# Optimization experiments

Measured on AMD Instinct MI355X. Metric: run time of the kernel, lower is better.

The kernel has to match this reference:

```python
import jax, jax.numpy as jnp
import numpy as np

B, S, D, O, E = 8, 4096, 1024, 1024, 64

def setup_inputs() -> dict:
    key = jax.random.key(0)
    kx, kgw, kgb, kew, keb = jax.random.split(key, 5)
    x = jax.random.normal(kx, (B, S, D), dtype=jnp.float32)
    gate_w = jax.random.normal(kgw, (E, D), dtype=jnp.float32) * 0.02
    gate_b = jnp.zeros((E,), dtype=jnp.float32)
    expert_w = jax.random.normal(kew, (E, D, O), dtype=jnp.float32) * 0.02
    expert_b = jnp.zeros((E, O), dtype=jnp.float32)
    return {"x": x, "gate_w": gate_w, "gate_b": gate_b,
            "expert_w": expert_w, "expert_b": expert_b}

def reference(x, gate_w, gate_b, expert_w, expert_b):
    # x: [B,S,D] -> flatten tokens. With world_size=1 the all-reduce and
    # all-to-alls in the torch module are identities, and per-chunk processing
    # is token-independent, so one global pass is mathematically identical.
    b, s, d = x.shape
    xt = x.reshape(-1, d)                                   # [N, D]
    logits = xt @ gate_w.T + gate_b                         # [N, E]
    gates = jax.nn.softmax(logits, axis=-1)
    sel = jnp.argmax(gates, axis=-1)                        # [N] top-1 expert
    order = jnp.argsort(sel)                                # stable sort by expert
    xs = xt[order]                                          # tokens grouped by expert
    counts = jnp.bincount(sel, length=E).astype(jnp.int32)  # tokens per expert
    # Grouped expert GEMM: row block e of xs multiplies expert_w[e].
    ys = jax.lax.ragged_dot(xs, expert_w, counts)           # [N, O]
    ys = ys + expert_b[sel[order]]
    # Combine: scatter sorted outputs back to original token positions.
    # (Note: torch output is NOT scaled by gate probability.)
    out = jnp.zeros((xt.shape[0], expert_w.shape[-1]), dtype=ys.dtype)
    out = out.at[order].set(ys)
    return out.reshape(b, s, -1)
```

## Files before the change

### kernel.cpp

```cpp
#include <hip/hip_runtime.h>
#include <hip/hip_bf16.h>

#define N_TOK 32768
#define DIM 1024
#define OUTD 1024
#define NEXP 64

typedef __attribute__((ext_vector_type(4))) float f32x4;
typedef __attribute__((ext_vector_type(8))) short bf16x8;

__device__ __forceinline__ unsigned short f2bf(float f) {
    unsigned int u = __builtin_bit_cast(unsigned int, f);
    u += 0x7FFFu + ((u >> 16) & 1u);
    return (unsigned short)(u >> 16);
}

__device__ __forceinline__ uint4 pack8(float4 a, float4 b) {
    uint4 p;
    p.x = (unsigned int)f2bf(a.x) | ((unsigned int)f2bf(a.y) << 16);
    p.y = (unsigned int)f2bf(a.z) | ((unsigned int)f2bf(a.w) << 16);
    p.z = (unsigned int)f2bf(b.x) | ((unsigned int)f2bf(b.y) << 16);
    p.w = (unsigned int)f2bf(b.z) | ((unsigned int)f2bf(b.w) << 16);
    return p;
}

__device__ __forceinline__ float4 ntload4(const float* p) {
    f32x4 v = __builtin_nontemporal_load(reinterpret_cast<const f32x4*>(p));
    float4 r; r.x = v[0]; r.y = v[1]; r.z = v[2]; r.w = v[3];
    return r;
}

#define GLOAD16(gp, lp) \
    __builtin_amdgcn_global_load_lds((const __attribute__((address_space(1))) void*)(gp), \
                                     (__attribute__((address_space(3))) void*)(lp), 16, 0, 0)

__global__ __launch_bounds__(256) void prep_kernel(const float* __restrict__ x,
        const float* __restrict__ gw, const float* __restrict__ gb,
        const float* __restrict__ ew,
        int* __restrict__ sel, int* __restrict__ nflag, int* __restrict__ flags,
        int* __restrict__ counts,
        unsigned short* __restrict__ xb, unsigned short* __restrict__ wt)
{
    __shared__ __align__(16) char smem[18688];
    int tid = threadIdx.x;

    if (blockIdx.x < 512) {
        unsigned short* Ag = (unsigned short*)smem;
        unsigned short* Bg = (unsigned short*)(smem + 8192);
        int* h = (int*)(smem + 16384);
        if (tid < NEXP) h[tid] = 0;

        int t0 = blockIdx.x * 64;
        int lane = tid & 63;
        int w = tid >> 6;
        int lr = lane & 15, lg = lane >> 4;

        int rowS = tid >> 2;
        int koffS = (((tid & 3) ^ ((tid >> 3) & 3)) * 8);
        const float* xsrc = x + (size_t)(t0 + rowS) * DIM + koffS;
        const float* wsrc = gw + (size_t)rowS * DIM + koffS;
        unsigned short* xdst = xb ? xb + (size_t)(t0 + rowS) * DIM + koffS : nullptr;

        f32x4 acc[4];
#pragma unroll
        for (int n = 0; n < 4; n++)
#pragma unroll
            for (int c = 0; c < 4; c++) acc[n][c] = 0.f;

        float4 v0 = *reinterpret_cast<const float4*>(xsrc);
        float4 v1 = *reinterpret_cast<const float4*>(xsrc + 4);
        float4 v2 = *reinterpret_cast<const float4*>(wsrc);
        float4 v3 = *reinterpret_cast<const float4*>(wsrc + 4);
        {
            uint4 pa = pack8(v0, v1), pb = pack8(v2, v3);
            *reinterpret_cast<uint4*>(&Ag[tid * 8]) = pa;
            *reinterpret_cast<uint4*>(&Bg[tid * 8]) = pb;
            if (xdst) *reinterpret_cast<uint4*>(xdst) = pa;
        }
        __syncthreads();

        const char* Agc = (const char*)Ag;
        const char* Bgc = (const char*)Bg;
        int fko = (lg ^ ((lr >> 1) & 3)) * 16;

#pragma unroll 1
        for (int t = 0; t < 32; ++t) {
            if (t < 31) {
                int k0 = (t + 1) * 32;
                v0 = *reinterpret_cast<const float4*>(xsrc + k0);
                v1 = *reinterpret_cast<const float4*>(xsrc + k0 + 4);
                v2 = *reinterpret_cast<const float4*>(wsrc + k0);
                v3 = *reinterpret_cast<const float4*>(wsrc + k0 + 4);
            }
            int boff = (t & 1) * 4096;
            bf16x8 afr = *reinterpret_cast<const bf16x8*>(Agc + boff + ((w * 16 + lr) << 6) + fko);
#pragma unroll
            for (int n = 0; n < 4; n++) {
                bf16x8 bfr = *reinterpret_cast<const bf16x8*>(Bgc + boff + ((n * 16 + lr) << 6) + fko);
                acc[n] = __builtin_amdgcn_mfma_f32_16x16x32_bf16(afr, bfr, acc[n], 0, 0, 0);
            }
            if (t < 31) {
                uint4 pa = pack8(v0, v1), pb = pack8(v2, v3);
                int soff = ((t + 1) & 1) * 2048;
                *reinterpret_cast<uint4*>(&Ag[soff + tid * 8]) = pa;
                *reinterpret_cast<uint4*>(&Bg[soff + tid * 8]) = pb;
                if (xdst) *reinterpret_cast<uint4*>(xdst + (t + 1) * 32) = pa;
            }
            __syncthreads();
        }

        float gbv[4];
#pragma unroll
        for (int n = 0; n < 4; n++) gbv[n] = gb[n * 16 + lr];
#pragma unroll
        for (int i = 0; i < 4; i++) {
            float m1 = -1e30f, m2 = -1e30f; int e1 = 0;
#pragma unroll
            for (int n = 0; n < 4; n++) {
                float v = acc[n][i] + gbv[n];
                if (v > m1) { m2 = m1; m1 = v; e1 = n * 16 + lr; }
                else if (v > m2) m2 = v;
            }
#pragma unroll
            for (int d = 1; d < 16; d <<= 1) {
                float om1 = __shfl_xor(m1, d, 16);
                float om2 = __shfl_xor(m2, d, 16);
                int   oe1 = __shfl_xor(e1, d, 16);
                if (om1 > m1 || (om1 == m1 && oe1 < e1)) {
                    m2 = fmaxf(om2, m1); m1 = om1; e1 = oe1;
                } else {
                    m2 = fmaxf(m2, om1);
                }
            }
            if (lr == 0) {
                int t = t0 + w * 16 + lg * 4 + i;
                sel[t] = e1;
                atomicAdd(&h[e1], 1);
                if (m1 - m2 < 0.01f) {
                    int idx = atomicAdd(nflag, 1);
                    if (idx < 16384) flags[idx] = t;
                }
            }
        }
        __syncthreads();
        if (tid < NEXP && h[tid]) atomicAdd(&counts[tid], h[tid]);
    } else {
        if (!wt) return;
        unsigned short* ts0 = (unsigned short*)smem;
        unsigned short* ts1 = (unsigned short*)(smem + 9216);
        int lin = blockIdx.x - 512;
        int e = lin >> 5;
        int d0 = ((lin >> 4) & 1) * 512;
        int o0 = (lin & 15) * 64;
        const float* src = ew + (size_t)e * (DIM * OUTD);
        unsigned short* dst = wt + (size_t)e * (DIM * OUTD);
        int og = tid & 7;
        int dl = tid >> 3;
        int dc = tid & 7;
        int ol = tid >> 3;

        float4 c0, c1, c2, c3;
        {
            const float* sr0 = &src[(size_t)(d0 + dl) * OUTD + o0 + og * 8];
            const float* sr1 = &src[(size_t)(d0 + dl + 32) * OUTD + o0 + og * 8];
            c0 = ntload4(sr0);
            c1 = ntload4(sr0 + 4);
            c2 = ntload4(sr1);
            c3 = ntload4(sr1 + 4);
        }
#pragma unroll
        for (int s = 0; s < 8; ++s) {
            float4 n0 = c0, n1 = c1, n2 = c2, n3 = c3;
            if (s < 7) {
                int dsn = d0 + (s + 1) * 64;
                const float* sr0 = &src[(size_t)(dsn + dl) * OUTD + o0 + og * 8];
                const float* sr1 = &src[(size_t)(dsn + dl + 32) * OUTD + o0 + og * 8];
                n0 = ntload4(sr0);
                n1 = ntload4(sr0 + 4);
                n2 = ntload4(sr1);
                n3 = ntload4(sr1 + 4);
            }
            unsigned short* tsb = (s & 1) ? ts1 : ts0;
#pragma unroll
            for (int half = 0; half < 2; ++half) {
                int dLoc = dl + 32 * half;
                float4 va = half ? c2 : c0;
                float4 vb = half ? c3 : c1;
                unsigned short b[8] = { f2bf(va.x), f2bf(va.y), f2bf(va.z), f2bf(va.w),
                                        f2bf(vb.x), f2bf(vb.y), f2bf(vb.z), f2bf(vb.w) };
                int dg = dLoc >> 3, dr = dLoc & 7;
#pragma unroll
                for (int k = 0; k < 8; k++) {
                    int o = og * 8 + k;
                    int key = (o & 7) ^ ((o >> 3) & 7);
                    tsb[o * 72 + ((dg ^ key) << 3) + dr] = b[k];
                }
            }
            __syncthreads();
            int ds0 = d0 + s * 64;
#pragma unroll
            for (int i = 0; i < 2; i++) {
                int o = ol + 32 * i;
                int key = (o & 7) ^ ((o >> 3) & 7);
                uint4 v = *reinterpret_cast<const uint4*>(&tsb[o * 72 + ((dc ^ key) << 3)]);
                *reinterpret_cast<uint4*>(&dst[(size_t)(o0 + o) * DIM + ds0 + dc * 8]) = v;
            }
            c0 = n0; c1 = n1; c2 = n2; c3 = n3;
        }
    }
}

__global__ __launch_bounds__(256) void gate_fix_kernel(const float* __restrict__ x,
        const float* __restrict__ gw, const float* __restrict__ gb,
        int* __restrict__ sel, const int* __restrict__ nflag, const int* __restrict__ flags,
        int* __restrict__ counts)
{
    __shared__ __align__(16) float xrow[4][DIM];
    int n = *nflag; if (n > 16384) n = 16384;
    int wv = threadIdx.x >> 6, lane = threadIdx.x & 63;
    int fi = blockIdx.x * 4 + wv;
    if (fi >= n) return;
    int t = flags[fi];

    const float4* xs4 = reinterpret_cast<const float4*>(x + (size_t)t * DIM);
    float4* xl4 = reinterpret_cast<float4*>(xrow[wv]);
#pragma unroll
    for (int i = 0; i < 4; i++)
        xl4[lane + i * 64] = xs4[lane + i * 64];

    const float4* wr4 = reinterpret_cast<const float4*>(gw + (size_t)lane * DIM);
    double a0 = 0, a1 = 0, a2 = 0, a3 = 0;
#pragma unroll 4
    for (int k = 0; k < DIM / 4; ++k) {
        float4 wv4 = wr4[k];
        float4 xv4 = xl4[k];
        a0 += (double)xv4.x * (double)wv4.x;
        a1 += (double)xv4.y * (double)wv4.y;
        a2 += (double)xv4.z * (double)wv4.z;
        a3 += (double)xv4.w * (double)wv4.w;
    }
    double m1 = ((a0 + a1) + (a2 + a3)) + (double)gb[lane];
    int e1 = lane;
#pragma unroll
    for (int d = 1; d < 64; d <<= 1) {
        double om1 = __shfl_xor(m1, d, 64);
        int   oe1  = __shfl_xor(e1, d, 64);
        if (om1 > m1 || (om1 == m1 && oe1 < e1)) { m1 = om1; e1 = oe1; }
    }
    if (lane == 0) {
        int eOld = sel[t];
        if (eOld != e1) {
            sel[t] = e1;
            atomicSub(&counts[eOld], 1);
            atomicAdd(&counts[e1], 1);
        }
    }
}

__global__ void sched_kernel(const int* __restrict__ counts, int* __restrict__ offsets,
                             int* __restrict__ schedE, int* __restrict__ schedR,
                             int* __restrict__ totalRB, int rowsShift)
{
    int e = threadIdx.x;
    int c = counts[e];
    int v = c;
#pragma unroll
    for (int d = 1; d < 64; d <<= 1) { int y = __shfl_up(v, d, 64); if (e >= d) v += y; }
    offsets[e] = v - c;
    if (e == 63) offsets[NEXP] = v;
    int rows = 1 << rowsShift;
    int nb = (c + rows - 1) >> rowsShift;
    int rbv = nb;
#pragma unroll
    for (int d = 1; d < 64; d <<= 1) { int y = __shfl_up(rbv, d, 64); if (e >= d) rbv += y; }
    int rbBase = rbv - nb;
    for (int i = 0; i < nb; i++) { schedE[rbBase + i] = e; schedR[rbBase + i] = i << rowsShift; }
    if (e == 63) *totalRB = rbv;
}

__global__ __launch_bounds__(256) void scatter_kernel(const int* __restrict__ sel,
        const int* __restrict__ offsets, int* __restrict__ cursor, int* __restrict__ perm)
{
    int t = blockIdx.x * 256 + threadIdx.x;
    int e = sel[t];
    int pos = offsets[e] + atomicAdd(&cursor[e], 1);
    perm[pos] = t;
}

__global__ __launch_bounds__(512, 4) void moe_gemm7(
        const unsigned short* __restrict__ xb, const unsigned short* __restrict__ wt,
        const float* __restrict__ eb,
        const int* __restrict__ perm, const int* __restrict__ offsets,
        const int* __restrict__ counts, const int* __restrict__ schedE,
        const int* __restrict__ schedR, const int* __restrict__ totalRB,
        float* __restrict__ out)
{
    int idx = blockIdx.x;
    int xcd = idx & 7;
    int s = idx >> 3;
    int cb = s & 7;
    int rb = (s >> 3) * 8 + xcd;
    if (rb >= *totalRB) return;
    int e = schedE[rb], r0 = schedR[rb];
    int cnt = counts[e], base = offsets[e];

    __shared__ __align__(16) unsigned short As[24576];
    __shared__ __align__(16) unsigned short Bs[12288];

    int tid = threadIdx.x;
    int lane = tid & 63;
    int wv = tid >> 6;
    int wr = wv >> 1, wc = wv & 1;
    int lr = lane & 15, lg = lane >> 4;

    int rowS = tid >> 2;
    int koff = ((tid & 3) ^ ((tid >> 3) & 3)) * 8;
    int rA1 = r0 + rowS, rA2 = r0 + 128 + rowS;
    int tokA1 = (rA1 < cnt) ? perm[base + rA1] : 0;
    int tokA2 = (rA2 < cnt) ? perm[base + rA2] : 0;

    const unsigned short* wte = wt + ((size_t)e << 20);
    const unsigned short* aSrc1 = xb + (size_t)tokA1 * DIM + koff;
    const unsigned short* aSrc2 = xb + (size_t)tokA2 * DIM + koff;
    const unsigned short* bSrc1 = wte + (size_t)(cb * 128 + rowS) * DIM + koff;

    unsigned short* AsQ0 = As + wv * 512;
    unsigned short* AsQ1 = As + 4096 + wv * 512;
    unsigned short* BsQ0 = Bs + wv * 512;

    f32x4 acc[4][4];
#pragma unroll
    for (int m = 0; m < 4; m++)
#pragma unroll
        for (int n = 0; n < 4; n++)
#pragma unroll
            for (int c = 0; c < 4; c++) acc[m][n][c] = 0.f;

    const char* Asc = (const char*)As;
    const char* Bsc = (const char*)Bs;
    int fko = (lg ^ ((lr >> 1) & 3)) * 16;

    auto stage = [&](int buf, int k0) {
        GLOAD16(aSrc1 + k0, AsQ0 + buf * 8192);
        GLOAD16(aSrc2 + k0, AsQ1 + buf * 8192);
        GLOAD16(bSrc1 + k0, BsQ0 + buf * 4096);
    };
    auto compute = [&](int buf) {
        int aoff = buf * 16384;
        int boff = buf * 8192;
        bf16x8 bfr[4];
#pragma unroll
        for (int n = 0; n < 4; n++) {
            int row = wc * 64 + n * 16 + lr;
            bfr[n] = *reinterpret_cast<const bf16x8*>(Bsc + boff + (row << 6) + fko);
        }
        __builtin_amdgcn_s_setprio(1);
#pragma unroll
        for (int m = 0; m < 4; m++) {
            int row = wr * 64 + m * 16 + lr;
            bf16x8 afr = *reinterpret_cast<const bf16x8*>(Asc + aoff + (row << 6) + fko);
#pragma unroll
            for (int n = 0; n < 4; n++)
                acc[m][n] = __builtin_amdgcn_mfma_f32_16x16x32_bf16(afr, bfr[n], acc[m][n], 0, 0, 0);
        }
        __builtin_amdgcn_s_setprio(0);
    };

    stage(0, 0);
    stage(1, 32);

    int cbuf = 0, sbuf = 2;
#pragma unroll 1
    for (int t = 0; t < 30; ++t) {
        asm volatile("s_waitcnt vmcnt(3)" ::: "memory");
        __builtin_amdgcn_s_barrier();
        stage(sbuf, (t + 2) * 32);
        compute(cbuf);
        cbuf = (cbuf == 2) ? 0 : cbuf + 1;
        sbuf = (sbuf == 2) ? 0 : sbuf + 1;
    }
    asm volatile("s_waitcnt vmcnt(3)" ::: "memory");
    __builtin_amdgcn_s_barrier();
    compute(cbuf);
    cbuf = (cbuf == 2) ? 0 : cbuf + 1;
    asm volatile("s_waitcnt vmcnt(0)" ::: "memory");
    __builtin_amdgcn_s_barrier();
    compute(cbuf);

    float bias[4];
#pragma unroll
    for (int n = 0; n < 4; n++)
        bias[n] = eb[e * OUTD + cb * 128 + wc * 64 + n * 16 + lr];
#pragma unroll
    for (int m = 0; m < 4; m++) {
        int rowLoc = wr * 64 + m * 16 + lg * 4;
#pragma unroll
        for (int i2 = 0; i2 < 4; i2++) {
            int r = r0 + rowLoc + i2;
            if (r < cnt) {
                int tk = perm[base + r];
                float* op = out + (size_t)tk * OUTD + cb * 128 + wc * 64 + lr;
#pragma unroll
                for (int n = 0; n < 4; n++)
                    __builtin_nontemporal_store(acc[m][n][i2] + bias[n], op + n * 16);
            }
        }
    }
}

extern "C" void kernel_launch(void* const* d_in, const int* in_sizes, int n_in,
                              void* d_out, int out_size, void* d_ws, size_t ws_size,
                              hipStream_t stream)
{
    const float* x  = (const float*)d_in[0];
    const float* gw = (const float*)d_in[1];
    const float* gb = (const float*)d_in[2];
    const float* ew = (const float*)d_in[3];
    const float* eb = (const float*)d_in[4];
    float* out = (float*)d_out;

    char* ws = (char*)d_ws;
    int* counts  = (int*)(ws + 0);
    int* cursor  = (int*)(ws + 256);
    int* offsets = (int*)(ws + 512);
    int* totalRB = (int*)(ws + 1024);
    int* nflag   = (int*)(ws + 1028);
    int* schedE  = (int*)(ws + 2048);
    int* schedR  = (int*)(ws + 4096);
    int* flags   = (int*)(ws + 8192);
    int* sel     = (int*)(ws + 131072);
    int* perm    = (int*)(ws + 262144);

    const size_t WT_OFF   = (size_t)1 << 20;
    const size_t WT_BYTES = (size_t)NEXP * DIM * OUTD * 2;
    const size_t XB_OFF   = WT_OFF + WT_BYTES;
    const size_t XB_BYTES = (size_t)N_TOK * DIM * 2;
    int mode = (ws_size >= XB_OFF + XB_BYTES) ? 2 : 0;
    unsigned short* wt = (mode == 2) ? (unsigned short*)(ws + WT_OFF) : nullptr;
    unsigned short* xb = (mode == 2) ? (unsigned short*)(ws + XB_OFF) : nullptr;

    hipMemsetAsync(ws, 0, 2048, stream);

    prep_kernel<<<dim3(512 + ((mode == 2) ? 2048 : 0)), 256, 0, stream>>>(
        x, gw, gb, ew, sel, nflag, flags, counts, xb, wt);
    gate_fix_kernel<<<dim3(4096), 256, 0, stream>>>(x, gw, gb, sel, nflag, flags, counts);
    sched_kernel<<<dim3(1), 64, 0, stream>>>(counts, offsets, schedE, schedR, totalRB, 8);
    scatter_kernel<<<dim3(N_TOK / 256), 256, 0, stream>>>(sel, offsets, cursor, perm);

    moe_gemm7<<<dim3(1536), 512, 0, stream>>>(xb, wt, eb, perm, offsets, counts,
                                              schedE, schedR, totalRB, out);
}
```

Before: 367.2 us.

## Enlarge GEMM block tile to 256x256 with 1024 threads and 4-stage pipeline

Doubles the output column tile per block to 256, using 16 waves in a 4x4 layout, so each A tile is reused across more columns and the grid shrinks. The LDS ring grows from three to four stages, with one A and one B load per thread per stage and adjusted wait counts. The larger LDS footprint limits each CU to one block, which reduces latency hiding across blocks and leaves fewer blocks to balance uneven expert sizes.

```diff
diff --git a/kernel.cpp b/kernel.cpp
--- a/kernel.cpp
+++ b/kernel.cpp
@@ -287,7 +287,7 @@
     perm[pos] = t;
 }
 
-__global__ __launch_bounds__(512, 4) void moe_gemm7(
+__global__ __launch_bounds__(1024, 4) void moe_gemm10(
         const unsigned short* __restrict__ xb, const unsigned short* __restrict__ wt,
         const float* __restrict__ eb,
         const int* __restrict__ perm, const int* __restrict__ offsets,
@@ -298,35 +298,31 @@
     int idx = blockIdx.x;
     int xcd = idx & 7;
     int s = idx >> 3;
-    int cb = s & 7;
-    int rb = (s >> 3) * 8 + xcd;
+    int cb = s & 3;
+    int rb = (s >> 2) * 8 + xcd;
     if (rb >= *totalRB) return;
     int e = schedE[rb], r0 = schedR[rb];
     int cnt = counts[e], base = offsets[e];
 
-    __shared__ __align__(16) unsigned short As[24576];
-    __shared__ __align__(16) unsigned short Bs[12288];
+    __shared__ __align__(16) unsigned short As[32768];
+    __shared__ __align__(16) unsigned short Bs[32768];
 
     int tid = threadIdx.x;
     int lane = tid & 63;
     int wv = tid >> 6;
-    int wr = wv >> 1, wc = wv & 1;
+    int wr = wv >> 2, wc = wv & 3;
     int lr = lane & 15, lg = lane >> 4;
 
     int rowS = tid >> 2;
     int koff = ((tid & 3) ^ ((tid >> 3) & 3)) * 8;
-    int rA1 = r0 + rowS, rA2 = r0 + 128 + rowS;
-    int tokA1 = (rA1 < cnt) ? perm[base + rA1] : 0;
-    int tokA2 = (rA2 < cnt) ? perm[base + rA2] : 0;
-
-    const unsigned short* wte = wt + ((size_t)e << 20);
-    const unsigned short* aSrc1 = xb + (size_t)tokA1 * DIM + koff;
-    const unsigned short* aSrc2 = xb + (size_t)tokA2 * DIM + koff;
-    const unsigned short* bSrc1 = wte + (size_t)(cb * 128 + rowS) * DIM + koff;
-
-    unsigned short* AsQ0 = As + wv * 512;
-    unsigned short* AsQ1 = As + 4096 + wv * 512;
-    unsigned short* BsQ0 = Bs + wv * 512;
+    int rA = r0 + rowS;
+    int tokA = (rA < cnt) ? perm[base + rA] : 0;
+    const unsigned short* aSrc = xb + (size_t)tokA * DIM + koff;
+    const unsigned short* bSrc = wt + ((size_t)e << 20)
+                               + (size_t)(cb * 256 + rowS) * DIM + koff;
+
+    unsigned short* AsQ = As + wv * 512;
+    unsigned short* BsQ = Bs + wv * 512;
 
     f32x4 acc[4][4];
 #pragma unroll
@@ -341,13 +337,11 @@
     int fko = (lg ^ ((lr >> 1) & 3)) * 16;
 
     auto stage = [&](int buf, int k0) {
-        GLOAD16(aSrc1 + k0, AsQ0 + buf * 8192);
-        GLOAD16(aSrc2 + k0, AsQ1 + buf * 8192);
-        GLOAD16(bSrc1 + k0, BsQ0 + buf * 4096);
+        GLOAD16(aSrc + k0, AsQ + buf * 8192);
+        GLOAD16(bSrc + k0, BsQ + buf * 8192);
     };
     auto compute = [&](int buf) {
-        int aoff = buf * 16384;
-        int boff = buf * 8192;
+        int boff = buf * 16384;
         bf16x8 bfr[4];
 #pragma unroll
         for (int n = 0; n < 4; n++) {
@@ -358,7 +352,7 @@
 #pragma unroll
         for (int m = 0; m < 4; m++) {
             int row = wr * 64 + m * 16 + lr;
-            bf16x8 afr = *reinterpret_cast<const bf16x8*>(Asc + aoff + (row << 6) + fko);
+            bf16x8 afr = *reinterpret_cast<const bf16x8*>(Asc + boff + (row << 6) + fko);
 #pragma unroll
             for (int n = 0; n < 4; n++)
                 acc[m][n] = __builtin_amdgcn_mfma_f32_16x16x32_bf16(afr, bfr[n], acc[m][n], 0, 0, 0);
@@ -368,29 +362,29 @@
 
     stage(0, 0);
     stage(1, 32);
-
-    int cbuf = 0, sbuf = 2;
+    stage(2, 64);
+
 #pragma unroll 1
-    for (int t = 0; t < 30; ++t) {
-        asm volatile("s_waitcnt vmcnt(3)" ::: "memory");
+    for (int t = 0; t < 29; ++t) {
+        asm volatile("s_waitcnt vmcnt(4)" ::: "memory");
         __builtin_amdgcn_s_barrier();
-        stage(sbuf, (t + 2) * 32);
-        compute(cbuf);
-        cbuf = (cbuf == 2) ? 0 : cbuf + 1;
-        sbuf = (sbuf == 2) ? 0 : sbuf + 1;
-    }
-    asm volatile("s_waitcnt vmcnt(3)" ::: "memory");
+        stage((t + 3) & 3, (t + 3) * 32);
+        compute(t & 3);
+    }
+    asm volatile("s_waitcnt vmcnt(4)" ::: "memory");
     __builtin_amdgcn_s_barrier();
-    compute(cbuf);
-    cbuf = (cbuf == 2) ? 0 : cbuf + 1;
+    compute(29 & 3);
+    asm volatile("s_waitcnt vmcnt(2)" ::: "memory");
+    __builtin_amdgcn_s_barrier();
+    compute(30 & 3);
     asm volatile("s_waitcnt vmcnt(0)" ::: "memory");
     __builtin_amdgcn_s_barrier();
-    compute(cbuf);
+    compute(31 & 3);
 
     float bias[4];
 #pragma unroll
     for (int n = 0; n < 4; n++)
-        bias[n] = eb[e * OUTD + cb * 128 + wc * 64 + n * 16 + lr];
+        bias[n] = eb[e * OUTD + cb * 256 + wc * 64 + n * 16 + lr];
 #pragma unroll
     for (int m = 0; m < 4; m++) {
         int rowLoc = wr * 64 + m * 16 + lg * 4;
@@ -399,7 +393,7 @@
             int r = r0 + rowLoc + i2;
             if (r < cnt) {
                 int tk = perm[base + r];
-                float* op = out + (size_t)tk * OUTD + cb * 128 + wc * 64 + lr;
+                float* op = out + (size_t)tk * OUTD + cb * 256 + wc * 64 + lr;
 #pragma unroll
                 for (int n = 0; n < 4; n++)
                     __builtin_nontemporal_store(acc[m][n][i2] + bias[n], op + n * 16);
@@ -447,6 +441,6 @@
     sched_kernel<<<dim3(1), 64, 0, stream>>>(counts, offsets, schedE, schedR, totalRB, 8);
     scatter_kernel<<<dim3(N_TOK / 256), 256, 0, stream>>>(sel, offsets, cursor, perm);
 
-    moe_gemm7<<<dim3(1536), 512, 0, stream>>>(xb, wt, eb, perm, offsets, counts,
-                                              schedE, schedR, totalRB, out);
-}
+    moe_gemm10<<<dim3(1024), 1024, 0, stream>>>(xb, wt, eb, perm, offsets, counts,
+                                                schedE, schedR, totalRB, out);
+}
```

After: 376.3 us. +2.5%, slower.
